# Kernel tuning notes

Measured on AMD Instinct MI355X. Metric: run time of the kernel, lower is better.

## Reference

```python
import jax, jax.numpy as jnp
import numpy as np

B, S, I, H, A = 512, 256, 12, 256, 9


def _lstm_layer(x, w_ih, w_hh, b_ih, b_hh):
    # x: [B,S,in] -> outputs [B,S,H], final (h, c). PyTorch gate order i,f,g,o.
    b, s, _ = x.shape
    h_dim = w_hh.shape[1]
    xg = jnp.einsum('bsi,gi->bsg', x, w_ih) + b_ih  # [B,S,4H] precomputed input gates

    def step(carry, xg_t):
        h, c = carry
        gates = xg_t + h @ w_hh.T + b_hh
        i_g, f_g, g_g, o_g = jnp.split(gates, 4, axis=-1)
        c = jax.nn.sigmoid(f_g) * c + jax.nn.sigmoid(i_g) * jnp.tanh(g_g)
        h = jax.nn.sigmoid(o_g) * jnp.tanh(c)
        return (h, c), h

    init = (jnp.zeros((b, h_dim), x.dtype), jnp.zeros((b, h_dim), x.dtype))
    (h, c), ys = jax.lax.scan(step, init, jnp.swapaxes(xg, 0, 1))
    return jnp.swapaxes(ys, 0, 1), h, c


def setup_inputs() -> dict:
    key = jax.random.key(0)
    ks = jax.random.split(key, 20)
    sc = 0.1
    inp = {
        'x': jax.random.normal(ks[0], (B, S, I), jnp.float32),
        'mask': jnp.ones((B, A), jnp.float32),
        'W_emb': jax.random.normal(ks[1], (H, I), jnp.float32) * sc,
        'b_emb': jnp.zeros((H,), jnp.float32),
        'w_ih0': jax.random.normal(ks[2], (4 * H, H), jnp.float32) * sc,
        'w_hh0': jax.random.normal(ks[3], (4 * H, H), jnp.float32) * sc,
        'b_ih0': jnp.zeros((4 * H,), jnp.float32),
        'b_hh0': jnp.zeros((4 * H,), jnp.float32),
        'w_ih1': jax.random.normal(ks[4], (4 * H, H), jnp.float32) * sc,
        'w_hh1': jax.random.normal(ks[5], (4 * H, H), jnp.float32) * sc,
        'b_ih1': jnp.zeros((4 * H,), jnp.float32),
        'b_hh1': jnp.zeros((4 * H,), jnp.float32),
        'ln_g': jnp.ones((H,), jnp.float32),
        'ln_b': jnp.zeros((H,), jnp.float32),
        'w1': jax.random.normal(ks[6], (32, H), jnp.float32) * sc,
        'b1': jnp.zeros((32,), jnp.float32),
        'w2': jax.random.normal(ks[7], (A, 32), jnp.float32) * sc,
        'b2': jnp.zeros((A,), jnp.float32),
    }
    return inp


def reference(x, mask, W_emb, b_emb, w_ih0, w_hh0, b_ih0, b_hh0,
              w_ih1, w_hh1, b_ih1, b_hh1, ln_g, ln_b, w1, b1, w2, b2):
    # embed + ReLU
    emb = jax.nn.relu(jnp.einsum('bsi,hi->bsh', x, W_emb) + b_emb)  # [B,S,H]
    # 2-layer LSTM (dropout between layers is identity in eval mode)
    y0, h0, c0 = _lstm_layer(emb, w_ih0, w_hh0, b_ih0, b_hh0)
    y1, h1, c1 = _lstm_layer(y0, w_ih1, w_hh1, b_ih1, b_hh1)
    last = y1[:, -1, :]  # [B,H]
    # LayerNorm
    mu = jnp.mean(last, axis=-1, keepdims=True)
    var = jnp.mean((last - mu) ** 2, axis=-1, keepdims=True)
    normed = (last - mu) / jnp.sqrt(var + 1e-5) * ln_g + ln_b
    # MLP head (dropout identity in eval)
    hdn = jax.nn.relu(normed @ w1.T + b1)
    logits = hdn @ w2.T + b2  # [B,A]
    logits = logits + (1.0 - mask) * -1e9
    hidden = (jnp.stack([h0, h1]), jnp.stack([c0, c1]))
    return logits, hidden
```

## Files before the change

### kernel.cpp

```cpp
#include <hip/hip_runtime.h>
#include <cstdint>
#include <cstddef>

typedef __attribute__((ext_vector_type(8))) short short8;
typedef __attribute__((ext_vector_type(4))) float f32x4;

#define MFMA16(a, b, c) __builtin_amdgcn_mfma_f32_16x16x32_bf16((a), (b), (c), 0, 0, 0)

constexpr int kB = 512, kS = 256, kI = 12, kH = 256, kA = 9;
constexpr int kNS = 8;
constexpr int kNB = 32;
constexpr int kT  = 512;
constexpr int LDH = 264;
constexpr int LDG = 132;
constexpr int kBH = kB * kH;
constexpr int FLS = 512;

constexpr int OUT_H = kB * kA;
constexpr int OUT_C = OUT_H + 2 * kBH;

__device__ __forceinline__ short f2bf(float f) {
  uint32_t u = __float_as_uint(f);
  u += 0x7fffu + ((u >> 16) & 1u);
  return (short)(u >> 16);
}
__device__ __forceinline__ float fast_sigmoid(float v) {
  return __builtin_amdgcn_rcpf(1.f + __expf(-v));
}
__device__ __forceinline__ float fast_tanh(float v) {
  return 2.f * __builtin_amdgcn_rcpf(1.f + __expf(-2.f * v)) - 1.f;
}

__global__ __launch_bounds__(kT) void lstm_scan_kernel(
    const float* __restrict__ x,
    const float* __restrict__ W_emb, const float* __restrict__ b_emb,
    const float* __restrict__ w_ih0, const float* __restrict__ w_hh0,
    const float* __restrict__ b_ih0, const float* __restrict__ b_hh0,
    const float* __restrict__ w_ih1, const float* __restrict__ w_hh1,
    const float* __restrict__ b_ih1, const float* __restrict__ b_hh1,
    unsigned short* __restrict__ h0ex, unsigned short* __restrict__ h1ex,
    int* __restrict__ flags,
    float* __restrict__ dout)
{
  const int tid   = threadIdx.x;
  const int btile = blockIdx.x & (kNB - 1);
  const int slice = blockIdx.x >> 5;
  const int b0    = btile * 16;
  const int lane  = tid & 63;
  const int wave  = tid >> 6;
  const int n16   = lane & 15;
  const int quad  = lane >> 4;

  __shared__ short embL[16 * LDH];
  __shared__ short hA[16 * LDH];
  __shared__ short hB[16 * LDH];
  __shared__ float gL0[16 * LDG];
  __shared__ float gL1[16 * LDG];

  for (int i = tid; i < 16 * LDH; i += kT) { hA[i] = 0; hB[i] = 0; }

  const float* Wm[4] = { w_ih0, w_hh0, w_ih1, w_hh1 };
  short8 wB[4][8];
  {
    const int gcol = (wave >> 1) * kH + slice * 32 + (wave & 1) * 16 + n16;
#pragma unroll
    for (int mat = 0; mat < 4; ++mat) {
      const float* wp = Wm[mat] + (size_t)gcol * kH;
#pragma unroll
      for (int kk = 0; kk < 8; ++kk) {
        const float* p = wp + kk * 32 + quad * 8;
        const float4 f0 = *(const float4*)p;
        const float4 f1 = *(const float4*)(p + 4);
        short8 v;
        v[0] = f2bf(f0.x); v[1] = f2bf(f0.y); v[2] = f2bf(f0.z); v[3] = f2bf(f0.w);
        v[4] = f2bf(f1.x); v[5] = f2bf(f1.y); v[6] = f2bf(f1.z); v[7] = f2bf(f1.w);
        wB[mat][kk] = v;
      }
    }
  }
  short8 wE[2];
  float bembv[2];
#pragma unroll
  for (int i = 0; i < 2; ++i) {
    const int col = wave * 32 + i * 16 + n16;
    short8 v;
#pragma unroll
    for (int j = 0; j < 8; ++j) {
      const int k = quad * 8 + j;
      v[j] = (k < kI) ? f2bf(W_emb[col * kI + k]) : (short)0;
    }
    wE[i] = v;
    bembv[i] = b_emb[col];
  }
  const int erow = tid >> 5;
  const int ec   = tid & 31;
  const int ecol = slice * 32 + ec;
  float bi0[4], bi1[4];
#pragma unroll
  for (int g = 0; g < 4; ++g) {
    bi0[g] = b_ih0[g * kH + ecol] + b_hh0[g * kH + ecol];
    bi1[g] = b_ih1[g * kH + ecol] + b_hh1[g * kH + ecol];
  }
  float c0v = 0.f, c1v = 0.f;

  {
    const float* xr = x + (size_t)(b0 + n16) * kS * kI;
    short8 xa;
#pragma unroll
    for (int j = 0; j < 8; ++j) {
      const int k = quad * 8 + j;
      xa[j] = (k < kI) ? f2bf(xr[k]) : (short)0;
    }
#pragma unroll
    for (int i = 0; i < 2; ++i) {
      f32x4 z = {0.f, 0.f, 0.f, 0.f};
      f32x4 e = MFMA16(xa, wE[i], z);
      const int col = wave * 32 + i * 16 + n16;
#pragma unroll
      for (int r = 0; r < 4; ++r) {
        float v = e[r] + bembv[i];
        v = v > 0.f ? v : 0.f;
        embL[(quad * 4 + r) * LDH + col] = f2bf(v);
      }
    }
  }
  __syncthreads();

  int* const fl = flags + btile * FLS;

  for (int p = 0; p <= kS; ++p) {
    const int par = p & 1;

    {
      f32x4 a0 = {0.f,0.f,0.f,0.f}, g1 = a0;
#pragma unroll
      for (int kk = 0; kk < 8; ++kk) {
        const short8 ha = *(const short8*)&hA[n16 * LDH + kk * 32 + quad * 8];
        a0 = MFMA16(ha, wB[1][kk], a0);
        g1 = MFMA16(ha, wB[2][kk], g1);
      }
#pragma unroll
      for (int kk = 0; kk < 8; ++kk) {
        const short8 e = *(const short8*)&embL[n16 * LDH + kk * 32 + quad * 8];
        a0 = MFMA16(e, wB[0][kk], a0);
      }
#pragma unroll
      for (int kk = 0; kk < 8; ++kk) {
        const short8 hb = *(const short8*)&hB[n16 * LDH + kk * 32 + quad * 8];
        g1 = MFMA16(hb, wB[3][kk], g1);
      }
      const int lcol = (wave >> 1) * 32 + (wave & 1) * 16 + n16;
#pragma unroll
      for (int r = 0; r < 4; ++r) {
        gL0[(quad * 4 + r) * LDG + lcol] = a0[r];
        gL1[(quad * 4 + r) * LDG + lcol] = g1[r];
      }
    }
    __syncthreads();

    if (p < kS) {
      const float iv = gL0[erow * LDG +       ec] + bi0[0];
      const float fv = gL0[erow * LDG +  32 + ec] + bi0[1];
      const float gv = gL0[erow * LDG +  64 + ec] + bi0[2];
      const float ov = gL0[erow * LDG +  96 + ec] + bi0[3];
      const float c = fast_sigmoid(fv) * c0v + fast_sigmoid(iv) * fast_tanh(gv);
      c0v = c;
      const float h = fast_sigmoid(ov) * fast_tanh(c);
      unsigned short* dst = &h0ex[(size_t)par * kBH + (size_t)(b0 + erow) * kH + ecol];
      __hip_atomic_store(dst, (unsigned short)f2bf(h), __ATOMIC_RELAXED, __HIP_MEMORY_SCOPE_AGENT);
      if (p == kS - 1) {
        dout[OUT_H + (size_t)(b0 + erow) * kH + ecol] = h;
        dout[OUT_C + (size_t)(b0 + erow) * kH + ecol] = c;
      }
    }
    if (p >= 1) {
      const float iv = gL1[erow * LDG +       ec] + bi1[0];
      const float fv = gL1[erow * LDG +  32 + ec] + bi1[1];
      const float gv = gL1[erow * LDG +  64 + ec] + bi1[2];
      const float ov = gL1[erow * LDG +  96 + ec] + bi1[3];
      const float c = fast_sigmoid(fv) * c1v + fast_sigmoid(iv) * fast_tanh(gv);
      c1v = c;
      const float h = fast_sigmoid(ov) * fast_tanh(c);
      unsigned short* dst = &h1ex[(size_t)par * kBH + (size_t)(b0 + erow) * kH + ecol];
      __hip_atomic_store(dst, (unsigned short)f2bf(h), __ATOMIC_RELAXED, __HIP_MEMORY_SCOPE_AGENT);
      if (p == kS) {
        dout[OUT_H + kBH + (size_t)(b0 + erow) * kH + ecol] = h;
        dout[OUT_C + kBH + (size_t)(b0 + erow) * kH + ecol] = c;
      }
    }
    __syncthreads();

    if (p < kS) {
      if (tid == 0)
        __hip_atomic_fetch_add(fl + p, 1, __ATOMIC_RELAXED, __HIP_MEMORY_SCOPE_AGENT);

      if (p + 1 < kS) {
        const float* xr = x + ((size_t)(b0 + n16) * kS + (p + 1)) * kI;
        short8 xa;
#pragma unroll
        for (int j = 0; j < 8; ++j) {
          const int k = quad * 8 + j;
          xa[j] = (k < kI) ? f2bf(xr[k]) : (short)0;
        }
#pragma unroll
        for (int i = 0; i < 2; ++i) {
          f32x4 z = {0.f, 0.f, 0.f, 0.f};
          f32x4 e = MFMA16(xa, wE[i], z);
          const int col = wave * 32 + i * 16 + n16;
#pragma unroll
          for (int r = 0; r < 4; ++r) {
            float v = e[r] + bembv[i];
            v = v > 0.f ? v : 0.f;
            embL[(quad * 4 + r) * LDH + col] = f2bf(v);
          }
        }
      }

      while (__hip_atomic_load(fl + p, __ATOMIC_RELAXED, __HIP_MEMORY_SCOPE_AGENT) < kNS)
        __builtin_amdgcn_s_sleep(1);

      {
        const int rr = tid >> 5;
        const int cc = (tid & 31) * 8;
        const size_t base = (size_t)par * kBH + (size_t)(b0 + rr) * kH + cc;
        const uint64_t* s0 = (const uint64_t*)&h0ex[base];
        const uint64_t* s1 = (const uint64_t*)&h1ex[base];
        uint64_t va0 = __hip_atomic_load(s0 + 0, __ATOMIC_RELAXED, __HIP_MEMORY_SCOPE_AGENT);
        uint64_t va1 = __hip_atomic_load(s0 + 1, __ATOMIC_RELAXED, __HIP_MEMORY_SCOPE_AGENT);
        uint64_t vb0 = __hip_atomic_load(s1 + 0, __ATOMIC_RELAXED, __HIP_MEMORY_SCOPE_AGENT);
        uint64_t vb1 = __hip_atomic_load(s1 + 1, __ATOMIC_RELAXED, __HIP_MEMORY_SCOPE_AGENT);
        uint64_t* dA = (uint64_t*)&hA[rr * LDH + cc];
        uint64_t* dB = (uint64_t*)&hB[rr * LDH + cc];
        dA[0] = va0; dA[1] = va1;
        dB[0] = vb0; dB[1] = vb1;
      }
      __syncthreads();
    }
  }
}

__global__ __launch_bounds__(64) void head_kernel(
    const float* __restrict__ h1last, const float* __restrict__ mask,
    const float* __restrict__ ln_g, const float* __restrict__ ln_b,
    const float* __restrict__ w1, const float* __restrict__ b1,
    const float* __restrict__ w2, const float* __restrict__ b2,
    float* __restrict__ out)
{
  const int r = blockIdx.x;
  const int lane = threadIdx.x;
  __shared__ float ns[kH];
  __shared__ float hd[32];
  const float4 v = *(const float4*)&h1last[r * kH + lane * 4];
  float vv[4] = {v.x, v.y, v.z, v.w};
  float s = vv[0] + vv[1] + vv[2] + vv[3];
#pragma unroll
  for (int off = 32; off > 0; off >>= 1) s += __shfl_xor(s, off, 64);
  const float mean = s * (1.f / kH);
  float q = 0.f;
#pragma unroll
  for (int j = 0; j < 4; ++j) { const float d = vv[j] - mean; q += d * d; }
#pragma unroll
  for (int off = 32; off > 0; off >>= 1) q += __shfl_xor(q, off, 64);
  const float rstd = rsqrtf(q * (1.f / kH) + 1e-5f);
#pragma unroll
  for (int j = 0; j < 4; ++j) {
    const int c = lane * 4 + j;
    ns[c] = (vv[j] - mean) * rstd * ln_g[c] + ln_b[c];
  }
  __syncthreads();
  if (lane < 32) {
    float a = b1[lane];
    const float* wr = w1 + lane * kH;
    for (int k = 0; k < kH; ++k) a += ns[k] * wr[k];
    hd[lane] = a > 0.f ? a : 0.f;
  }
  __syncthreads();
  if (lane < kA) {
    float a = b2[lane];
    const float* wr = w2 + lane * 32;
#pragma unroll
    for (int k = 0; k < 32; ++k) a += hd[k] * wr[k];
    a += (1.f - mask[r * kA + lane]) * (-1e9f);
    out[r * kA + lane] = a;
  }
}

extern "C" void kernel_launch(void* const* d_in, const int* in_sizes, int n_in,
                              void* d_out, int out_size, void* d_ws, size_t ws_size,
                              hipStream_t stream)
{
  (void)in_sizes; (void)n_in; (void)out_size; (void)ws_size;
  const float* x     = (const float*)d_in[0];
  const float* mask  = (const float*)d_in[1];
  const float* W_emb = (const float*)d_in[2];
  const float* b_emb = (const float*)d_in[3];
  const float* w_ih0 = (const float*)d_in[4];
  const float* w_hh0 = (const float*)d_in[5];
  const float* b_ih0 = (const float*)d_in[6];
  const float* b_hh0 = (const float*)d_in[7];
  const float* w_ih1 = (const float*)d_in[8];
  const float* w_hh1 = (const float*)d_in[9];
  const float* b_ih1 = (const float*)d_in[10];
  const float* b_hh1 = (const float*)d_in[11];
  const float* ln_g  = (const float*)d_in[12];
  const float* ln_b  = (const float*)d_in[13];
  const float* w1    = (const float*)d_in[14];
  const float* b1    = (const float*)d_in[15];
  const float* w2    = (const float*)d_in[16];
  const float* b2    = (const float*)d_in[17];
  float* out = (float*)d_out;

  unsigned short* h0ex = (unsigned short*)d_ws;
  unsigned short* h1ex = h0ex + 2 * kBH;
  int* flags = (int*)(h1ex + 2 * kBH);
  const size_t flag_bytes = (size_t)kNB * FLS * sizeof(int);

  hipMemsetAsync(flags, 0, flag_bytes, stream);
  hipMemsetAsync(h1ex, 0, (size_t)kBH * sizeof(unsigned short), stream);

  lstm_scan_kernel<<<dim3(kNB * kNS), dim3(kT), 0, stream>>>(
      x, W_emb, b_emb, w_ih0, w_hh0, b_ih0, b_hh0, w_ih1, w_hh1, b_ih1, b_hh1,
      h0ex, h1ex, flags, out);

  head_kernel<<<dim3(kB), dim3(64), 0, stream>>>(
      out + OUT_H + kBH, mask, ln_g, ln_b, w1, b1, w2, b2, out);
}
```

Baseline: 966.1 us.

## Precompute next-step input projection during wait and use per-slice flags

The layer-0 input-gate MFMAs on the embedding tile for the next timestep are now computed while waiting on the cross-block barrier, and the result is carried into the next iteration's accumulator. The embedding tile is double-buffered two steps ahead, and its computation is interleaved between the global hidden-state loads and the LDS stores. The shared atomic counter is replaced by per-slice flag words that each block stores and a poller reads as 64-bit loads, removing contention on one counter. This costs extra registers and LDS and enlarges the flags buffer.

After: 1.018 ms. 5.4% more time.

```diff
diff --git a/kernel.cpp b/kernel.cpp
--- a/kernel.cpp
+++ b/kernel.cpp
@@ -14,7 +14,7 @@
 constexpr int LDH = 264;
 constexpr int LDG = 132;
 constexpr int kBH = kB * kH;
-constexpr int FLS = 512;
+constexpr int FLS = kS * kNS;
 
 constexpr int OUT_H = kB * kA;
 constexpr int OUT_C = OUT_H + 2 * kBH;
@@ -51,7 +51,7 @@
   const int n16   = lane & 15;
   const int quad  = lane >> 4;
 
-  __shared__ short embL[16 * LDH];
+  __shared__ short embL[2][16 * LDH];
   __shared__ short hA[16 * LDH];
   __shared__ short hB[16 * LDH];
   __shared__ float gL0[16 * LDG];
@@ -103,28 +103,38 @@
   }
   float c0v = 0.f, c1v = 0.f;
 
-  {
-    const float* xr = x + (size_t)(b0 + n16) * kS * kI;
-    short8 xa;
-#pragma unroll
-    for (int j = 0; j < 8; ++j) {
-      const int k = quad * 8 + j;
-      xa[j] = (k < kI) ? f2bf(xr[k]) : (short)0;
-    }
-#pragma unroll
-    for (int i = 0; i < 2; ++i) {
-      f32x4 z = {0.f, 0.f, 0.f, 0.f};
-      f32x4 e = MFMA16(xa, wE[i], z);
-      const int col = wave * 32 + i * 16 + n16;
-#pragma unroll
-      for (int r = 0; r < 4; ++r) {
-        float v = e[r] + bembv[i];
-        v = v > 0.f ? v : 0.f;
-        embL[(quad * 4 + r) * LDH + col] = f2bf(v);
-      }
-    }
-  }
+#define EMB_TILE(DST, T)                                                    \
+  {                                                                         \
+    const float* xr = x + ((size_t)(b0 + n16) * kS + (T)) * kI;             \
+    short8 xa;                                                              \
+    _Pragma("unroll")                                                       \
+    for (int j = 0; j < 8; ++j) {                                           \
+      const int k = quad * 8 + j;                                           \
+      xa[j] = (k < kI) ? f2bf(xr[k]) : (short)0;                            \
+    }                                                                       \
+    _Pragma("unroll")                                                       \
+    for (int i = 0; i < 2; ++i) {                                           \
+      f32x4 zz = {0.f, 0.f, 0.f, 0.f};                                      \
+      f32x4 e = MFMA16(xa, wE[i], zz);                                      \
+      const int col = wave * 32 + i * 16 + n16;                             \
+      _Pragma("unroll")                                                     \
+      for (int r = 0; r < 4; ++r) {                                         \
+        float v = e[r] + bembv[i];                                          \
+        v = v > 0.f ? v : 0.f;                                              \
+        (DST)[(quad * 4 + r) * LDH + col] = f2bf(v);                        \
+      }                                                                     \
+    }                                                                       \
+  }
+
+  EMB_TILE(embL[0], 0);
+  EMB_TILE(embL[1], 1);
   __syncthreads();
+  f32x4 zcur = {0.f, 0.f, 0.f, 0.f};
+#pragma unroll
+  for (int kk = 0; kk < 8; ++kk) {
+    const short8 e = *(const short8*)&embL[0][n16 * LDH + kk * 32 + quad * 8];
+    zcur = MFMA16(e, wB[0][kk], zcur);
+  }
 
   int* const fl = flags + btile * FLS;
 
@@ -132,17 +142,13 @@
     const int par = p & 1;
 
     {
-      f32x4 a0 = {0.f,0.f,0.f,0.f}, g1 = a0;
+      f32x4 a0 = zcur;
+      f32x4 g1 = {0.f, 0.f, 0.f, 0.f};
 #pragma unroll
       for (int kk = 0; kk < 8; ++kk) {
         const short8 ha = *(const short8*)&hA[n16 * LDH + kk * 32 + quad * 8];
         a0 = MFMA16(ha, wB[1][kk], a0);
         g1 = MFMA16(ha, wB[2][kk], g1);
-      }
-#pragma unroll
-      for (int kk = 0; kk < 8; ++kk) {
-        const short8 e = *(const short8*)&embL[n16 * LDH + kk * 32 + quad * 8];
-        a0 = MFMA16(e, wB[0][kk], a0);
       }
 #pragma unroll
       for (int kk = 0; kk < 8; ++kk) {
@@ -192,51 +198,54 @@
 
     if (p < kS) {
       if (tid == 0)
-        __hip_atomic_fetch_add(fl + p, 1, __ATOMIC_RELAXED, __HIP_MEMORY_SCOPE_AGENT);
-
-      if (p + 1 < kS) {
-        const float* xr = x + ((size_t)(b0 + n16) * kS + (p + 1)) * kI;
-        short8 xa;
-#pragma unroll
-        for (int j = 0; j < 8; ++j) {
-          const int k = quad * 8 + j;
-          xa[j] = (k < kI) ? f2bf(xr[k]) : (short)0;
+        __hip_atomic_store(fl + p * kNS + slice, p + 1,
+                           __ATOMIC_RELAXED, __HIP_MEMORY_SCOPE_AGENT);
+
+      f32x4 z = {0.f, 0.f, 0.f, 0.f};
+#pragma unroll
+      for (int kk = 0; kk < 8; ++kk) {
+        const short8 e = *(const short8*)&embL[par ^ 1][n16 * LDH + kk * 32 + quad * 8];
+        z = MFMA16(e, wB[0][kk], z);
+      }
+
+      {
+        const uint64_t* f64 = (const uint64_t*)(fl + p * kNS);
+        const int tgt = p + 1;
+        for (;;) {
+          uint64_t v0 = __hip_atomic_load(f64 + 0, __ATOMIC_RELAXED, __HIP_MEMORY_SCOPE_AGENT);
+          uint64_t v1 = __hip_atomic_load(f64 + 1, __ATOMIC_RELAXED, __HIP_MEMORY_SCOPE_AGENT);
+          uint64_t v2 = __hip_atomic_load(f64 + 2, __ATOMIC_RELAXED, __HIP_MEMORY_SCOPE_AGENT);
+          uint64_t v3 = __hip_atomic_load(f64 + 3, __ATOMIC_RELAXED, __HIP_MEMORY_SCOPE_AGENT);
+          if ((int)(v0 & 0xffffffffu) >= tgt && (int)(v0 >> 32) >= tgt &&
+              (int)(v1 & 0xffffffffu) >= tgt && (int)(v1 >> 32) >= tgt &&
+              (int)(v2 & 0xffffffffu) >= tgt && (int)(v2 >> 32) >= tgt &&
+              (int)(v3 & 0xffffffffu) >= tgt && (int)(v3 >> 32) >= tgt)
+            break;
+          __builtin_amdgcn_s_sleep(1);
         }
-#pragma unroll
-        for (int i = 0; i < 2; ++i) {
-          f32x4 z = {0.f, 0.f, 0.f, 0.f};
-          f32x4 e = MFMA16(xa, wE[i], z);
-          const int col = wave * 32 + i * 16 + n16;
-#pragma unroll
-          for (int r = 0; r < 4; ++r) {
-            float v = e[r] + bembv[i];
-            v = v > 0.f ? v : 0.f;
-            embL[(quad * 4 + r) * LDH + col] = f2bf(v);
-          }
-        }
-      }
-
-      while (__hip_atomic_load(fl + p, __ATOMIC_RELAXED, __HIP_MEMORY_SCOPE_AGENT) < kNS)
-        __builtin_amdgcn_s_sleep(1);
-
-      {
-        const int rr = tid >> 5;
-        const int cc = (tid & 31) * 8;
-        const size_t base = (size_t)par * kBH + (size_t)(b0 + rr) * kH + cc;
-        const uint64_t* s0 = (const uint64_t*)&h0ex[base];
-        const uint64_t* s1 = (const uint64_t*)&h1ex[base];
-        uint64_t va0 = __hip_atomic_load(s0 + 0, __ATOMIC_RELAXED, __HIP_MEMORY_SCOPE_AGENT);
-        uint64_t va1 = __hip_atomic_load(s0 + 1, __ATOMIC_RELAXED, __HIP_MEMORY_SCOPE_AGENT);
-        uint64_t vb0 = __hip_atomic_load(s1 + 0, __ATOMIC_RELAXED, __HIP_MEMORY_SCOPE_AGENT);
-        uint64_t vb1 = __hip_atomic_load(s1 + 1, __ATOMIC_RELAXED, __HIP_MEMORY_SCOPE_AGENT);
-        uint64_t* dA = (uint64_t*)&hA[rr * LDH + cc];
-        uint64_t* dB = (uint64_t*)&hB[rr * LDH + cc];
-        dA[0] = va0; dA[1] = va1;
-        dB[0] = vb0; dB[1] = vb1;
-      }
+      }
+
+      const int rr = tid >> 5;
+      const int cc = (tid & 31) * 8;
+      const size_t base = (size_t)par * kBH + (size_t)(b0 + rr) * kH + cc;
+      const uint64_t* s0 = (const uint64_t*)&h0ex[base];
+      const uint64_t* s1 = (const uint64_t*)&h1ex[base];
+      uint64_t va0 = __hip_atomic_load(s0 + 0, __ATOMIC_RELAXED, __HIP_MEMORY_SCOPE_AGENT);
+      uint64_t va1 = __hip_atomic_load(s0 + 1, __ATOMIC_RELAXED, __HIP_MEMORY_SCOPE_AGENT);
+      uint64_t vb0 = __hip_atomic_load(s1 + 0, __ATOMIC_RELAXED, __HIP_MEMORY_SCOPE_AGENT);
+      uint64_t vb1 = __hip_atomic_load(s1 + 1, __ATOMIC_RELAXED, __HIP_MEMORY_SCOPE_AGENT);
+
+      if (p + 2 < kS) EMB_TILE(embL[par], p + 2);
+
+      uint64_t* dA = (uint64_t*)&hA[rr * LDH + cc];
+      uint64_t* dB = (uint64_t*)&hB[rr * LDH + cc];
+      dA[0] = va0; dA[1] = va1;
+      dB[0] = vb0; dB[1] = vb1;
       __syncthreads();
-    }
-  }
+      zcur = z;
+    }
+  }
+#undef EMB_TILE
 }
 
 __global__ __launch_bounds__(64) void head_kernel(
```

## Split waves by layer and replace counter barrier with per-wave byte flags

Applied to the files above, without the earlier changes.

Each wave now computes gate columns for only one layer (two 16-column tiles), instead of both layers for one tile, so every wave issues the same number of MFMAs and reads only its own operand buffers. The block-wide syncthreads before publishing is dropped. The single atomic-add counter per step is replaced by per-wave byte flags that each wave sets after waiting on its own stores, and consumers poll 64 bytes with eight 64-bit loads. This is meant to cut the barrier and atomic serialization on the cross-block critical path each timestep, at the cost of a larger flag array, wider polling traffic, and reliance on relaxed ordering plus an explicit vmcnt wait for visibility.

Result: slower. 1.195 ms (+23.7%).

```diff
diff --git a/kernel.cpp b/kernel.cpp
--- a/kernel.cpp
+++ b/kernel.cpp
@@ -14,7 +14,6 @@
 constexpr int LDH = 264;
 constexpr int LDG = 132;
 constexpr int kBH = kB * kH;
-constexpr int FLS = 512;
 
 constexpr int OUT_H = kB * kA;
 constexpr int OUT_C = OUT_H + 2 * kBH;
@@ -39,7 +38,7 @@
     const float* __restrict__ w_ih1, const float* __restrict__ w_hh1,
     const float* __restrict__ b_ih1, const float* __restrict__ b_hh1,
     unsigned short* __restrict__ h0ex, unsigned short* __restrict__ h1ex,
-    int* __restrict__ flags,
+    unsigned char* __restrict__ flags,
     float* __restrict__ dout)
 {
   const int tid   = threadIdx.x;
@@ -50,6 +49,8 @@
   const int wave  = tid >> 6;
   const int n16   = lane & 15;
   const int quad  = lane >> 4;
+  const int L     = wave & 1;
+  const int P     = wave >> 1;
 
   __shared__ short embL[16 * LDH];
   __shared__ short hA[16 * LDH];
@@ -59,22 +60,27 @@
 
   for (int i = tid; i < 16 * LDH; i += kT) { hA[i] = 0; hB[i] = 0; }
 
-  const float* Wm[4] = { w_ih0, w_hh0, w_ih1, w_hh1 };
-  short8 wB[4][8];
+  const float* m0 = L ? w_ih1 : w_ih0;
+  const float* m1 = L ? w_hh1 : w_hh0;
+  short8 wB[2][2][8];
   {
-    const int gcol = (wave >> 1) * kH + slice * 32 + (wave & 1) * 16 + n16;
-#pragma unroll
-    for (int mat = 0; mat < 4; ++mat) {
-      const float* wp = Wm[mat] + (size_t)gcol * kH;
-#pragma unroll
-      for (int kk = 0; kk < 8; ++kk) {
-        const float* p = wp + kk * 32 + quad * 8;
-        const float4 f0 = *(const float4*)p;
-        const float4 f1 = *(const float4*)(p + 4);
-        short8 v;
-        v[0] = f2bf(f0.x); v[1] = f2bf(f0.y); v[2] = f2bf(f0.z); v[3] = f2bf(f0.w);
-        v[4] = f2bf(f1.x); v[5] = f2bf(f1.y); v[6] = f2bf(f1.z); v[7] = f2bf(f1.w);
-        wB[mat][kk] = v;
+    const float* Wm[2] = { m0, m1 };
+#pragma unroll
+    for (int m = 0; m < 2; ++m) {
+#pragma unroll
+      for (int t = 0; t < 2; ++t) {
+        const int gcol = P * kH + slice * 32 + t * 16 + n16;
+        const float* wp = Wm[m] + (size_t)gcol * kH;
+#pragma unroll
+        for (int kk = 0; kk < 8; ++kk) {
+          const float* p4 = wp + kk * 32 + quad * 8;
+          const float4 f0 = *(const float4*)p4;
+          const float4 f1 = *(const float4*)(p4 + 4);
+          short8 v;
+          v[0] = f2bf(f0.x); v[1] = f2bf(f0.y); v[2] = f2bf(f0.z); v[3] = f2bf(f0.w);
+          v[4] = f2bf(f1.x); v[5] = f2bf(f1.y); v[6] = f2bf(f1.z); v[7] = f2bf(f1.w);
+          wB[m][t][kk] = v;
+        }
       }
     }
   }
@@ -126,34 +132,35 @@
   }
   __syncthreads();
 
-  int* const fl = flags + btile * FLS;
+  unsigned char* const flB = flags + (size_t)btile * kS * 64;
+  const uint64_t kOnes = 0x0101010101010101ULL;
 
   for (int p = 0; p <= kS; ++p) {
     const int par = p & 1;
 
     {
-      f32x4 a0 = {0.f,0.f,0.f,0.f}, g1 = a0;
+      const short* op1 = L ? hA : embL;
+      const short* op2 = L ? hB : hA;
+      f32x4 aA = {0.f,0.f,0.f,0.f}, aB = aA;
 #pragma unroll
       for (int kk = 0; kk < 8; ++kk) {
-        const short8 ha = *(const short8*)&hA[n16 * LDH + kk * 32 + quad * 8];
-        a0 = MFMA16(ha, wB[1][kk], a0);
-        g1 = MFMA16(ha, wB[2][kk], g1);
+        const short8 e = *(const short8*)&op1[n16 * LDH + kk * 32 + quad * 8];
+        aA = MFMA16(e, wB[0][0][kk], aA);
+        aB = MFMA16(e, wB[0][1][kk], aB);
       }
 #pragma unroll
       for (int kk = 0; kk < 8; ++kk) {
-        const short8 e = *(const short8*)&embL[n16 * LDH + kk * 32 + quad * 8];
-        a0 = MFMA16(e, wB[0][kk], a0);
-      }
-#pragma unroll
-      for (int kk = 0; kk < 8; ++kk) {
-        const short8 hb = *(const short8*)&hB[n16 * LDH + kk * 32 + quad * 8];
-        g1 = MFMA16(hb, wB[3][kk], g1);
-      }
-      const int lcol = (wave >> 1) * 32 + (wave & 1) * 16 + n16;
+        const short8 e = *(const short8*)&op2[n16 * LDH + kk * 32 + quad * 8];
+        aA = MFMA16(e, wB[1][0][kk], aA);
+        aB = MFMA16(e, wB[1][1][kk], aB);
+      }
+      float* gldst = L ? gL1 : gL0;
+      const int colA = P * 32 + n16;
+      const int colB = colA + 16;
 #pragma unroll
       for (int r = 0; r < 4; ++r) {
-        gL0[(quad * 4 + r) * LDG + lcol] = a0[r];
-        gL1[(quad * 4 + r) * LDG + lcol] = g1[r];
+        gldst[(quad * 4 + r) * LDG + colA] = aA[r];
+        gldst[(quad * 4 + r) * LDG + colB] = aB[r];
       }
     }
     __syncthreads();
@@ -188,11 +195,13 @@
         dout[OUT_C + kBH + (size_t)(b0 + erow) * kH + ecol] = c;
       }
     }
-    __syncthreads();
 
     if (p < kS) {
-      if (tid == 0)
-        __hip_atomic_fetch_add(fl + p, 1, __ATOMIC_RELAXED, __HIP_MEMORY_SCOPE_AGENT);
+      asm volatile("s_waitcnt vmcnt(0)" ::: "memory");
+      if (lane == 0)
+        __hip_atomic_store(flB + (size_t)p * 64 + slice * 8 + wave,
+                           (unsigned char)1,
+                           __ATOMIC_RELAXED, __HIP_MEMORY_SCOPE_AGENT);
 
       if (p + 1 < kS) {
         const float* xr = x + ((size_t)(b0 + n16) * kS + (p + 1)) * kI;
@@ -216,8 +225,23 @@
         }
       }
 
-      while (__hip_atomic_load(fl + p, __ATOMIC_RELAXED, __HIP_MEMORY_SCOPE_AGENT) < kNS)
-        __builtin_amdgcn_s_sleep(1);
+      {
+        const uint64_t* f64 = (const uint64_t*)(flB + (size_t)p * 64);
+        for (;;) {
+          const uint64_t v0 = __hip_atomic_load(f64 + 0, __ATOMIC_RELAXED, __HIP_MEMORY_SCOPE_AGENT);
+          const uint64_t v1 = __hip_atomic_load(f64 + 1, __ATOMIC_RELAXED, __HIP_MEMORY_SCOPE_AGENT);
+          const uint64_t v2 = __hip_atomic_load(f64 + 2, __ATOMIC_RELAXED, __HIP_MEMORY_SCOPE_AGENT);
+          const uint64_t v3 = __hip_atomic_load(f64 + 3, __ATOMIC_RELAXED, __HIP_MEMORY_SCOPE_AGENT);
+          const uint64_t v4 = __hip_atomic_load(f64 + 4, __ATOMIC_RELAXED, __HIP_MEMORY_SCOPE_AGENT);
+          const uint64_t v5 = __hip_atomic_load(f64 + 5, __ATOMIC_RELAXED, __HIP_MEMORY_SCOPE_AGENT);
+          const uint64_t v6 = __hip_atomic_load(f64 + 6, __ATOMIC_RELAXED, __HIP_MEMORY_SCOPE_AGENT);
+          const uint64_t v7 = __hip_atomic_load(f64 + 7, __ATOMIC_RELAXED, __HIP_MEMORY_SCOPE_AGENT);
+          if (v0 == kOnes && v1 == kOnes && v2 == kOnes && v3 == kOnes &&
+              v4 == kOnes && v5 == kOnes && v6 == kOnes && v7 == kOnes)
+            break;
+          __builtin_amdgcn_s_sleep(1);
+        }
+      }
 
       {
         const int rr = tid >> 5;
@@ -312,8 +336,8 @@
 
   unsigned short* h0ex = (unsigned short*)d_ws;
   unsigned short* h1ex = h0ex + 2 * kBH;
-  int* flags = (int*)(h1ex + 2 * kBH);
-  const size_t flag_bytes = (size_t)kNB * FLS * sizeof(int);
+  unsigned char* flags = (unsigned char*)(h1ex + 2 * kBH);
+  const size_t flag_bytes = (size_t)kNB * kS * 64;
 
   hipMemsetAsync(flags, 0, flag_bytes, stream);
   hipMemsetAsync(h1ex, 0, (size_t)kBH * sizeof(unsigned short), stream);
```
